# Optimization experiments

Measured on AMD Instinct MI355X. Metric: run time of the kernel, lower is better.

Reference implementation:

```python
import jax, jax.numpy as jnp
import numpy as np

H = 128
R = 14
B = 2048
TYPES = ['operator', 'table', 'column', 'predicate', 'operation', 'literal', 'numeral']
SIZES = {'operator': 100000, 'table': 20000, 'column': 120000, 'predicate': 60000,
         'operation': 100000, 'literal': 50000, 'numeral': 50000}
FEAT = {'operator': 4, 'table': 2, 'column': 10, 'predicate': 4, 'operation': 8,
        'literal': 1, 'numeral': 1}
# (name, src_type, dst_type, num_edges), order matches edge_type_mapping in the torch module
EDGES = [('ei_scannedby', 'table', 'operator', 100000),
         ('ei_pred_filters', 'predicate', 'operator', 100000),
         ('ei_outputby', 'column', 'operator', 100000),
         ('ei_col_connects', 'column', 'operation', 100000),
         ('ei_calledby', 'operator', 'operator', 100000),
         ('ei_op_filters', 'operation', 'operator', 100000),
         ('ei_op_connects', 'operation', 'predicate', 100000),
         ('ei_lit_connects', 'literal', 'operation', 100000),
         ('ei_num_connects', 'numeral', 'operation', 100000),
         ('ei_lit_self', 'literal', 'literal', 50000),
         ('ei_num_self', 'numeral', 'numeral', 50000),
         ('ei_tab_self', 'table', 'table', 20000),
         ('ei_col_self', 'column', 'column', 120000),
         ('ei_pred_self', 'predicate', 'predicate', 60000)]
OFFS = {}
_o = 0
for _t in TYPES:
    OFFS[_t] = _o
    _o += SIZES[_t]
N_TOTAL = _o


def setup_inputs():
    key = jax.random.key(0)
    ks = iter(jax.random.split(key, 64))
    inp = {}
    for t in TYPES:
        inp['x_' + t] = jax.random.normal(next(ks), (SIZES[t], FEAT[t]), jnp.float32)
    for name, s, d, E in EDGES:
        src = jax.random.randint(next(ks), (E,), 0, SIZES[s], jnp.int32)
        dst = jax.random.randint(next(ks), (E,), 0, SIZES[d], jnp.int32)
        inp[name] = jnp.stack([src, dst])
    inp['batch_operator'] = jnp.sort(
        jax.random.randint(next(ks), (SIZES['operator'],), 0, B, jnp.int32))

    def lin_w(k, din, dout):
        s = 1.0 / float(np.sqrt(din))
        return jax.random.uniform(k, (din, dout), jnp.float32, -s, s)

    for t in TYPES:
        inp['W_' + t] = lin_w(next(ks), FEAT[t], H)
        inp['b_' + t] = jnp.zeros((H,), jnp.float32)
    for c in ('c1', 'c2'):
        inp[c + '_root'] = lin_w(next(ks), H, H)
        inp[c + '_rel'] = jax.random.normal(next(ks), (R, H, H), jnp.float32) / float(np.sqrt(H))
        inp[c + '_bias'] = jnp.zeros((H,), jnp.float32)
    inp['n1_g'] = jnp.ones((H,), jnp.float32); inp['n1_b'] = jnp.zeros((H,), jnp.float32)
    inp['n2_g'] = jnp.ones((H,), jnp.float32); inp['n2_b'] = jnp.zeros((H,), jnp.float32)
    inp['W_lin'] = lin_w(next(ks), H, 1)
    inp['b_lin'] = jnp.zeros((1,), jnp.float32)
    return inp


def layer_norm(x, g, b, eps=1e-5):
    mu = jnp.mean(x, axis=-1, keepdims=True)
    var = jnp.var(x, axis=-1, keepdims=True)
    return (x - mu) * jax.lax.rsqrt(var + eps) * g + b


def rgcn(x, rel_edges, w_root, w_rel, bias):
    # PyG RGCNConv: root transform + per-relation gather -> GEMM -> scatter-mean into dst
    out = x @ w_root
    for r, (src, dst) in enumerate(rel_edges):
        msg = x[src] @ w_rel[r]  # [E_r, H]
        agg = jax.ops.segment_sum(msg, dst, num_segments=N_TOTAL)
        cnt = jax.ops.segment_sum(jnp.ones(src.shape, x.dtype), dst, num_segments=N_TOTAL)
        out = out + agg / jnp.maximum(cnt, 1.0)[:, None]
    return out + bias


def reference(x_operator, x_table, x_column, x_predicate, x_operation, x_literal, x_numeral,
              ei_scannedby, ei_pred_filters, ei_outputby, ei_col_connects, ei_calledby,
              ei_op_filters, ei_op_connects, ei_lit_connects, ei_num_connects, ei_lit_self,
              ei_num_self, ei_tab_self, ei_col_self, ei_pred_self, batch_operator,
              W_operator, b_operator, W_table, b_table, W_column, b_column,
              W_predicate, b_predicate, W_operation, b_operation, W_literal, b_literal,
              W_numeral, b_numeral, c1_root, c1_rel, c1_bias, c2_root, c2_rel, c2_bias,
              n1_g, n1_b, n2_g, n2_b, W_lin, b_lin):
    # per-node-type input embedding, then concat in fixed type order
    x = jnp.concatenate([
        x_operator @ W_operator + b_operator,
        x_table @ W_table + b_table,
        x_column @ W_column + b_column,
        x_predicate @ W_predicate + b_predicate,
        x_operation @ W_operation + b_operation,
        x_literal @ W_literal + b_literal,
        x_numeral @ W_numeral + b_numeral], axis=0)
    eis = [ei_scannedby, ei_pred_filters, ei_outputby, ei_col_connects, ei_calledby,
           ei_op_filters, ei_op_connects, ei_lit_connects, ei_num_connects, ei_lit_self,
           ei_num_self, ei_tab_self, ei_col_self, ei_pred_self]
    rel_edges = [(e[0] + OFFS[s], e[1] + OFFS[d]) for e, (_, s, d, _) in zip(eis, EDGES)]
    h = rgcn(x, rel_edges, c1_root, c1_rel, c1_bias)
    h = layer_norm(jax.nn.elu(h), n1_g, n1_b)  # dropout is identity in eval mode
    h = rgcn(h, rel_edges, c2_root, c2_rel, c2_bias)
    h = layer_norm(jax.nn.elu(h), n2_g, n2_b)
    op = h[:SIZES['operator']]  # operator offset is 0
    cnt = jax.ops.segment_sum(jnp.ones((op.shape[0],), op.dtype), batch_operator, num_segments=B)
    pooled = jax.ops.segment_sum(op, batch_operator, num_segments=B) / jnp.maximum(cnt, 1.0)[:, None]
    return (pooled @ W_lin + b_lin)[:, 0]  # [B]
```

## Files before the change

kernel.cpp:

```cpp
#include <hip/hip_runtime.h>
#include <hip/hip_bf16.h>
#include <math.h>

#define HD 128
#define N_OP 100000
#define N_L1 400000
#define NB 2048
#define CNT_TOT 1160000
#define EDG_TOT 1100000

typedef short short8 __attribute__((ext_vector_type(8)));
typedef float floatx4 __attribute__((ext_vector_type(4)));

static const int REL_E[14]    = {100000,100000,100000,100000,100000,100000,100000,100000,100000,50000,50000,20000,120000,60000};
static const int REL_DSZ[14]  = {100000,100000,100000,100000,100000,100000,60000,100000,100000,50000,50000,20000,120000,60000};
static const int CNT_OFF[14]  = {0,100000,200000,300000,400000,500000,600000,660000,760000,860000,910000,960000,980000,1100000};
static const int SRC_T[14] = {1,3,2,2,0,4,4,5,6,5,6,1,2,3};
static const int TF[7]  = {4,2,10,4,8,1,1};
static const size_t AGR_OFF[14] = {0,200000,600000,1600000,2600000,3000000,3800000,4280000,4380000,0,0,4480000,4520000,5720000};
#define AGR_TOT 5960000
static const int RELW[14] = {4,7,12,93,23,28,70,104,106,-1,-1,40,54,79};
static const int RELI[14] = {6,11,22,103,27,36,78,105,107,-1,-1,42,64,83};
static const int ROOTW[5] = {0,38,44,66,85};
static const int ROOTB[5] = {37,43,65,84,108};
#define WL1_ROWS 109

__device__ inline unsigned short f2bf(float f) {
  union { float f; unsigned int u; } v; v.f = f;
  unsigned int r = v.u + 0x7FFF + ((v.u >> 16) & 1);
  return (unsigned short)(r >> 16);
}
__device__ inline float bfu2f(unsigned short u) {
  union { unsigned int i; float f; } v; v.i = ((unsigned int)u) << 16; return v.f;
}

struct CJob { const int* dst; int coff; int E; int blk0; };
struct CombJob { const float* A; const float* bin; const float* Mtx; const float* extra; float* Wout; float* bout; int F; };
struct PrepPack {
  CJob j[12];
  int bblk0;
  int wstart;
  const int* batch; float* pcnt; int nop;
  CombJob c[17];
};

__global__ void prep_k(PrepPack P, const float* __restrict__ c2root,
                       const float* __restrict__ c2rel, __hip_bfloat16* __restrict__ Wt,
                       int* __restrict__ ICNT) {
  int b = blockIdx.x;
  if (b >= P.wstart) {
    int wj = b - P.wstart;
    if (wj < 17) {
      if (threadIdx.x >= 128) return;
      CombJob J = P.c[wj];
      int c = threadIdx.x;
      for (int f = 0; f <= J.F; ++f) {
        const float* arow = (f < J.F) ? &J.A[f * HD] : J.bin;
        float s = (f < J.F) ? 0.f : (J.extra ? J.extra[c] : 0.f);
        for (int k = 0; k < HD; ++k) s = fmaf(arow[k], J.Mtx[k * HD + c], s);
        if (f < J.F) J.Wout[f * HD + c] = s;
        else J.bout[c] = s;
      }
    } else {
      const int RID[6] = {-1, 0, 1, 2, 4, 5};
      int j = wj - 17;
      const float* W = (j == 0) ? c2root : (c2rel + (size_t)RID[j] * HD * HD);
      __hip_bfloat16* o = Wt + (size_t)j * 16384;
      for (int i = threadIdx.x; i < 16384; i += 256) {
        int i8 = i & 7;
        int ln = (i >> 3) & 63;
        int k4 = (i >> 9) & 3;
        int nt = i >> 11;
        int ln15 = ln & 15, quad = ln >> 4;
        int k = k4 * 32 + quad * 8 + i8;
        int n = nt * 16 + ln15;
        o[i] = __float2bfloat16(W[k * 128 + n]);
      }
    }
    return;
  }
  if (b >= P.bblk0) {
    int i = (b - P.bblk0) * 256 + threadIdx.x;
    if (i < P.nop) atomicAdd(&P.pcnt[P.batch[i]], 1.0f);
    return;
  }
  int ji = 0;
#pragma unroll
  for (int i = 1; i < 12; ++i) if (b >= P.j[i].blk0) ji = i;
  CJob J = P.j[ji];
  int e = (b - J.blk0) * 256 + threadIdx.x;
  if (e < J.E) atomicAdd(&ICNT[J.coff + J.dst[e]], 1);
}

#define SCAN_BLK 1024
__global__ void scan1(const int* __restrict__ in, int* __restrict__ out,
                      int* __restrict__ bsum, int n) {
  __shared__ int sh[256];
  int t = threadIdx.x;
  int base = blockIdx.x * SCAN_BLK + t * 4;
  int v0 = 0, v1 = 0, v2 = 0, v3 = 0;
  if (base + 3 < n) { int4 q = *(const int4*)&in[base]; v0 = q.x; v1 = q.y; v2 = q.z; v3 = q.w; }
  else {
    if (base < n) v0 = in[base];
    if (base + 1 < n) v1 = in[base + 1];
    if (base + 2 < n) v2 = in[base + 2];
    if (base + 3 < n) v3 = in[base + 3];
  }
  int ts = v0 + v1 + v2 + v3;
  sh[t] = ts; __syncthreads();
  for (int o = 1; o < 256; o <<= 1) {
    int x = (t >= o) ? sh[t - o] : 0;
    __syncthreads();
    sh[t] += x;
    __syncthreads();
  }
  int excl = sh[t] - ts;
  if (base < n) out[base] = excl;
  if (base + 1 < n) out[base + 1] = excl + v0;
  if (base + 2 < n) out[base + 2] = excl + v0 + v1;
  if (base + 3 < n) out[base + 3] = excl + v0 + v1 + v2;
  if (t == 255) bsum[blockIdx.x] = sh[255];
}

__global__ void scan3b(int* __restrict__ CUR, int2* __restrict__ OFF2,
                       const int* __restrict__ ICNT, const int* __restrict__ bs, int n) {
  __shared__ int sh[4];
  const int j = blockIdx.x, t = threadIdx.x;
  int s = 0;
  for (int i = t; i < j; i += 256) s += bs[i];
#pragma unroll
  for (int m = 32; m >= 1; m >>= 1) s += __shfl_xor(s, m, 64);
  if ((t & 63) == 0) sh[t >> 6] = s;
  __syncthreads();
  int base = sh[0] + sh[1] + sh[2] + sh[3];
  int i0 = j * SCAN_BLK + t * 4;
#pragma unroll
  for (int k = 0; k < 4; ++k) {
    int i = i0 + k;
    if (i < n) {
      int o = CUR[i] + base;
      CUR[i] = o;
      OFF2[i] = make_int2(o, ICNT[i]);
    }
  }
}

struct FJob { const int* src; const int* dst; int coff; int E; int blk0; };
struct FPackK { FJob j[12]; };

__global__ void fill_k(FPackK P, int* __restrict__ CUR, int* __restrict__ EDG) {
  int b = blockIdx.x;
  int ji = 0;
#pragma unroll
  for (int i = 1; i < 12; ++i) if (b >= P.j[i].blk0) ji = i;
  FJob J = P.j[ji];
  int e = (b - J.blk0) * 256 + threadIdx.x;
  if (e < J.E) {
    int pos = atomicAdd(&CUR[J.coff + J.dst[e]], 1);
    EDG[pos] = J.src[e];
  }
}

struct GJob { const float* x; float* agr; int coff; int D; int F; int blk0; };
struct GPack { GJob j[12]; };

template <int F>
__device__ inline void gathF(const float* __restrict__ x, float* __restrict__ agr,
                             const int* __restrict__ EDG, int2 oc, int d) {
  if (oc.y == 0) return;
  float s[F];
#pragma unroll
  for (int f = 0; f < F; ++f) s[f] = 0.f;
  for (int e = 0; e < oc.y; ++e) {
    int si = EDG[oc.x + e];
    const float* xp = &x[(size_t)si * F];
    if (F == 1) {
      s[0] += xp[0];
    } else if (F == 2) {
      float2 v = *(const float2*)xp; s[0] += v.x; s[1] += v.y;
    } else if (F == 4) {
      float4 v = *(const float4*)xp;
      s[0] += v.x; s[1] += v.y; s[2] += v.z; s[3] += v.w;
    } else if (F == 8) {
      float4 v0 = *(const float4*)xp, v1 = *(const float4*)(xp + 4);
      s[0] += v0.x; s[1] += v0.y; s[2] += v0.z; s[3] += v0.w;
      s[4] += v1.x; s[5] += v1.y; s[6] += v1.z; s[7] += v1.w;
    } else {
#pragma unroll
      for (int j = 0; j < F / 2; ++j) {
        float2 v = *(const float2*)(xp + 2 * j);
        s[2 * j] += v.x; s[2 * j + 1] += v.y;
      }
    }
  }
  float rc = 1.0f / (float)oc.y;
#pragma unroll
  for (int f = 0; f < F; ++f) s[f] *= rc;
  float* ap = &agr[(size_t)d * F];
  if (F == 1) { ap[0] = s[0]; }
  else if (F == 2) { *(float2*)ap = make_float2(s[0], s[1]); }
  else if (F == 4) { *(float4*)ap = make_float4(s[0], s[1], s[2], s[3]); }
  else if (F == 8) {
    *(float4*)ap = make_float4(s[0], s[1], s[2], s[3]);
    *(float4*)(ap + 4) = make_float4(s[4], s[5], s[6], s[7]);
  } else {
#pragma unroll
    for (int j = 0; j < F / 2; ++j)
      *(float2*)(ap + 2 * j) = make_float2(s[2 * j], s[2 * j + 1]);
  }
}

__global__ void gather_all(GPack P, const int2* __restrict__ OFF2, const int* __restrict__ EDG) {
  int b = blockIdx.x;
  int ji = 0;
#pragma unroll
  for (int i = 1; i < 12; ++i) if (b >= P.j[i].blk0) ji = i;
  GJob J = P.j[ji];
  int d = (b - J.blk0) * 256 + threadIdx.x;
  if (d >= J.D) return;
  int2 oc = OFF2[J.coff + d];
  switch (J.F) {
    case 1:  gathF<1>(J.x, J.agr, EDG, oc, d); break;
    case 2:  gathF<2>(J.x, J.agr, EDG, oc, d); break;
    case 4:  gathF<4>(J.x, J.agr, EDG, oc, d); break;
    case 8:  gathF<8>(J.x, J.agr, EDG, oc, d); break;
    default: gathF<10>(J.x, J.agr, EDG, oc, d); break;
  }
}

struct L1v2 {
  const float* x0; const float* x1; const float* x2; const float* x3; const float* x4;
  const float* AGR; const float* WL1; const int2* OFF2;
  const float* g; const float* b;
  unsigned short* Hb;
};

__device__ inline void ldv2(float* s, const float* __restrict__ p) {
  float2 v = *(const float2*)p; s[0] = v.x; s[1] = v.y;
}
__device__ inline void ldv4(float* s, const float* __restrict__ p) {
  float4 v = *(const float4*)p; s[0] = v.x; s[1] = v.y; s[2] = v.z; s[3] = v.w;
}
__device__ inline void relF1(float* s, const float* __restrict__ agr,
                             const int2* __restrict__ OFF2, int cb, int row) {
  if (OFF2[cb + row].y > 0) { s[0] = agr[row]; s[1] = 1.f; }
  else { s[0] = 0.f; s[1] = 0.f; }
}
__device__ inline void relF2(float* s, const float* __restrict__ agr,
                             const int2* __restrict__ OFF2, int cb, int row) {
  if (OFF2[cb + row].y > 0) { ldv2(s, &agr[(size_t)row * 2]); s[2] = 1.f; }
  else { s[0] = s[1] = s[2] = 0.f; }
}
__device__ inline void relF4(float* s, const float* __restrict__ agr,
                             const int2* __restrict__ OFF2, int cb, int row) {
  if (OFF2[cb + row].y > 0) { ldv4(s, &agr[(size_t)row * 4]); s[4] = 1.f; }
  else {
#pragma unroll
    for (int f = 0; f < 5; ++f) s[f] = 0.f;
  }
}
__device__ inline void relF8(float* s, const float* __restrict__ agr,
                             const int2* __restrict__ OFF2, int cb, int row) {
  if (OFF2[cb + row].y > 0) {
    ldv4(s, &agr[(size_t)row * 8]); ldv4(s + 4, &agr[(size_t)row * 8 + 4]); s[8] = 1.f;
  } else {
#pragma unroll
    for (int f = 0; f < 9; ++f) s[f] = 0.f;
  }
}
__device__ inline void relF10(float* s, const float* __restrict__ agr,
                              const int2* __restrict__ OFF2, int cb, int row) {
  if (OFF2[cb + row].y > 0) {
    const float* p = &agr[(size_t)row * 10];
#pragma unroll
    for (int j = 0; j < 5; ++j) ldv2(s + 2 * j, p + 2 * j);
    s[10] = 1.f;
  } else {
#pragma unroll
    for (int f = 0; f < 11; ++f) s[f] = 0.f;
  }
}

template <int KT>
__device__ inline void l1_dot8(const float* __restrict__ Ls, const float (&s)[KT],
                               int c4, float (&a)[8]) {
  {
    float4 w0 = *(const float4*)&Ls[KT * 128 + c4];
    float4 w1 = *(const float4*)&Ls[KT * 128 + c4 + 64];
    a[0] = w0.x; a[1] = w0.y; a[2] = w0.z; a[3] = w0.w;
    a[4] = w1.x; a[5] = w1.y; a[6] = w1.z; a[7] = w1.w;
  }
#pragma unroll
  for (int k = 0; k < KT; ++k) {
    float4 w0 = *(const float4*)&Ls[k * 128 + c4];
    float4 w1 = *(const float4*)&Ls[k * 128 + c4 + 64];
    a[0] = fmaf(s[k], w0.x, a[0]); a[1] = fmaf(s[k], w0.y, a[1]);
    a[2] = fmaf(s[k], w0.z, a[2]); a[3] = fmaf(s[k], w0.w, a[3]);
    a[4] = fmaf(s[k], w1.x, a[4]); a[5] = fmaf(s[k], w1.y, a[5]);
    a[6] = fmaf(s[k], w1.z, a[6]); a[7] = fmaf(s[k], w1.w, a[7]);
  }
}

__device__ inline void l1_fin8(float (&a)[8], int c4, const float* __restrict__ g,
                               const float* __restrict__ bb,
                               unsigned short* __restrict__ Hb, int orow) {
  float p = 0.f, q = 0.f;
#pragma unroll
  for (int j = 0; j < 8; ++j) {
    a[j] = (a[j] > 0.f) ? a[j] : (expf(a[j]) - 1.f);
    p += a[j]; q += a[j] * a[j];
  }
#pragma unroll
  for (int m = 8; m >= 1; m >>= 1) {
    p += __shfl_xor(p, m, 64);
    q += __shfl_xor(q, m, 64);
  }
  float mean = p * (1.0f / HD);
  float var = q * (1.0f / HD) - mean * mean;
  float rstd = rsqrtf(var + 1e-5f);
  float4 g0 = *(const float4*)&g[c4], g1 = *(const float4*)&g[c4 + 64];
  float4 b0 = *(const float4*)&bb[c4], b1 = *(const float4*)&bb[c4 + 64];
  float gg[8] = {g0.x, g0.y, g0.z, g0.w, g1.x, g1.y, g1.z, g1.w};
  float bv[8] = {b0.x, b0.y, b0.z, b0.w, b1.x, b1.y, b1.z, b1.w};
  float o[8];
#pragma unroll
  for (int j = 0; j < 8; ++j) o[j] = (a[j] - mean) * rstd * gg[j] + bv[j];
  uint2 lo, hi;
  lo.x = (unsigned int)f2bf(o[0]) | ((unsigned int)f2bf(o[1]) << 16);
  lo.y = (unsigned int)f2bf(o[2]) | ((unsigned int)f2bf(o[3]) << 16);
  hi.x = (unsigned int)f2bf(o[4]) | ((unsigned int)f2bf(o[5]) << 16);
  hi.y = (unsigned int)f2bf(o[6]) | ((unsigned int)f2bf(o[7]) << 16);
  *(uint2*)&Hb[(size_t)orow * HD + c4] = lo;
  *(uint2*)&Hb[(size_t)orow * HD + c4 + 64] = hi;
}

__global__ __launch_bounds__(256) void layer1_v5(L1v2 A) {
  __shared__ float Ls[38 * 128];
  const int b = blockIdx.x, t = threadIdx.x;
  const int wv = t >> 6, ln = t & 63;
  const int sub = ln >> 4, c4 = (ln & 15) * 4;
  int type, seg;
  if (b < 1563) { type = 0; seg = b; }
  else if (b < 1876) { type = 1; seg = b - 1563; }
  else if (b < 3751) { type = 2; seg = b - 1876; }
  else if (b < 4689) { type = 3; seg = b - 3751; }
  else { type = 4; seg = b - 4689; }
  const int NR[5] = {38, 6, 22, 19, 24};
  const int RB[5] = {0, 38, 44, 66, 85};
  const int TR[5] = {100000, 20000, 120000, 60000, 100000};
  const int OB[5] = {0, 100000, 120000, 240000, 300000};
  {
    const float4* src = (const float4*)(A.WL1 + RB[type] * 128);
    float4* dst = (float4*)Ls;
    int n4 = NR[type] * 32;
    for (int i = t; i < n4; i += 256) dst[i] = src[i];
  }
  __syncthreads();
  const int row0 = seg * 64, M = TR[type], ob = OB[type];

  if (type == 0) {
#pragma unroll
    for (int it = 0; it < 4; ++it) {
      int row = row0 + it * 16 + wv * 4 + sub;
      if (row >= M) continue;
      float s[37];
      ldv4(s, &A.x0[(size_t)row * 4]);
      relF2(s + 4, A.AGR + 0, A.OFF2, 0, row);
      relF4(s + 7, A.AGR + 200000, A.OFF2, 100000, row);
      relF10(s + 12, A.AGR + 600000, A.OFF2, 200000, row);
      relF4(s + 23, A.AGR + 2600000, A.OFF2, 400000, row);
      relF8(s + 28, A.AGR + 3000000, A.OFF2, 500000, row);
      float a[8];
      l1_dot8<37>(Ls, s, c4, a);
      l1_fin8(a, c4, A.g, A.b, A.Hb, ob + row);
    }
  } else if (type == 1) {
#pragma unroll
    for (int it = 0; it < 4; ++it) {
      int row = row0 + it * 16 + wv * 4 + sub;
      if (row >= M) continue;
      float s[5];
      ldv2(s, &A.x1[(size_t)row * 2]);
      relF2(s + 2, A.AGR + 4480000, A.OFF2, 960000, row);
      float a[8];
      l1_dot8<5>(Ls, s, c4, a);
      l1_fin8(a, c4, A.g, A.b, A.Hb, ob + row);
    }
  } else if (type == 2) {
#pragma unroll
    for (int it = 0; it < 4; ++it) {
      int row = row0 + it * 16 + wv * 4 + sub;
      if (row >= M) continue;
      float s[21];
      const float* p = &A.x2[(size_t)row * 10];
#pragma unroll
      for (int j = 0; j < 5; ++j) ldv2(s + 2 * j, p + 2 * j);
      relF10(s + 10, A.AGR + 4520000, A.OFF2, 980000, row);
      float a[8];
      l1_dot8<21>(Ls, s, c4, a);
      l1_fin8(a, c4, A.g, A.b, A.Hb, ob + row);
    }
  } else if (type == 3) {
#pragma unroll
    for (int it = 0; it < 4; ++it) {
      int row = row0 + it * 16 + wv * 4 + sub;
      if (row >= M) continue;
      float s[18];
      ldv4(s, &A.x3[(size_t)row * 4]);
      relF8(s + 4, A.AGR + 3800000, A.OFF2, 600000, row);
      relF4(s + 13, A.AGR + 5720000, A.OFF2, 1100000, row);
      float a[8];
      l1_dot8<18>(Ls, s, c4, a);
      l1_fin8(a, c4, A.g, A.b, A.Hb, ob + row);
    }
  } else {
#pragma unroll
    for (int it = 0; it < 4; ++it) {
      int row = row0 + it * 16 + wv * 4 + sub;
      if (row >= M) continue;
      float s[23];
      ldv4(s, &A.x4[(size_t)row * 8]);
      ldv4(s + 4, &A.x4[(size_t)row * 8 + 4]);
      relF10(s + 8, A.AGR + 1600000, A.OFF2, 300000, row);
      relF1(s + 19, A.AGR + 4280000, A.OFF2, 660000, row);
      relF1(s + 21, A.AGR + 4380000, A.OFF2, 760000, row);
      float a[8];
      l1_dot8<23>(Ls, s, c4, a);
      l1_fin8(a, c4, A.g, A.b, A.Hb, ob + row);
    }
  }
}

__global__ __launch_bounds__(256, 4)
void l2_fused(const unsigned short* __restrict__ Hb, const unsigned short* __restrict__ Wt,
              const int2* __restrict__ OFF2, const int* __restrict__ EDG,
              const float* __restrict__ c2bias, const float* __restrict__ n2g,
              const float* __restrict__ n2b, const float* __restrict__ Wl,
              const int* __restrict__ batch, float* __restrict__ accb, int M) {
  const int CSR_OFF[5] = {0, 100000, 200000, 400000, 500000};
  const int SOFF[5]    = {100000, 240000, 120000, 0, 300000};
  const int t = threadIdx.x, wv = t >> 6, ln = t & 63;
  const int quad = ln >> 4, ln15 = ln & 15, q8 = quad * 8;
  const int m0 = blockIdx.x * 64;
  const int rowA = m0 + wv * 16 + ln15;

  int2 ocs[5];
#pragma unroll
  for (int r = 0; r < 5; ++r)
    ocs[r] = (rowA < M) ? OFF2[CSR_OFF[r] + rowA] : make_int2(0, 0);
  int pre[5];
#pragma unroll
  for (int r = 0; r < 5; ++r)
    pre[r] = (ocs[r].y > 0) ? EDG[ocs[r].x] : 0;

  float bias_c[8], gw[8];
  float pg = 0.f, pb = 0.f;
#pragma unroll
  for (int nt = 0; nt < 8; ++nt) {
    int col = nt * 16 + ln15;
    float wl = Wl[col], gc = n2g[col], bc = n2b[col];
    bias_c[nt] = c2bias[col];
    gw[nt] = gc * wl;
    pg += gc * wl;
    pb += bc * wl;
  }
#pragma unroll
  for (int m = 8; m >= 1; m >>= 1) {
    pg += __shfl_xor(pg, m, 64);
    pb += __shfl_xor(pb, m, 64);
  }

  floatx4 acc[8];
#pragma unroll
  for (int b = 0; b < 8; ++b) acc[b] = (floatx4){0.f, 0.f, 0.f, 0.f};

  short8 nbuf[4];
  if (rowA < M) {
#pragma unroll
    for (int k4 = 0; k4 < 4; ++k4)
      nbuf[k4] = *(const short8*)&Hb[(size_t)rowA * HD + k4 * 32 + q8];
  } else {
#pragma unroll
    for (int k4 = 0; k4 < 4; ++k4)
#pragma unroll
      for (int j = 0; j < 8; ++j) nbuf[k4][j] = 0;
  }

#pragma unroll
  for (int term = 0; term < 6; ++term) {
    short8 afr[4];
#pragma unroll
    for (int k4 = 0; k4 < 4; ++k4) afr[k4] = nbuf[k4];

    if (term < 5) {
      int2 ocn = ocs[term];
      if (ocn.y > 0) {
        size_t s = (size_t)(pre[term] + SOFF[term]);
#pragma unroll
        for (int k4 = 0; k4 < 4; ++k4)
          nbuf[k4] = *(const short8*)&Hb[s * HD + k4 * 32 + q8];
      } else {
#pragma unroll
        for (int k4 = 0; k4 < 4; ++k4)
#pragma unroll
          for (int j = 0; j < 8; ++j) nbuf[k4][j] = 0;
      }
    }

    if (term > 0) {
      int2 oc = ocs[term - 1];
      if (oc.y > 1) {
        float sum[4][8];
#pragma unroll
        for (int k4 = 0; k4 < 4; ++k4)
#pragma unroll
          for (int j = 0; j < 8; ++j) sum[k4][j] = bfu2f((unsigned short)afr[k4][j]);
        int so = SOFF[term - 1];
        for (int e = 1; e < oc.y; ++e) {
          size_t s = (size_t)(EDG[oc.x + e] + so);
#pragma unroll
          for (int k4 = 0; k4 < 4; ++k4) {
            short8 h = *(const short8*)&Hb[s * HD + k4 * 32 + q8];
#pragma unroll
            for (int j = 0; j < 8; ++j) sum[k4][j] += bfu2f((unsigned short)h[j]);
          }
        }
        float rc = 1.0f / (float)oc.y;
#pragma unroll
        for (int k4 = 0; k4 < 4; ++k4)
#pragma unroll
          for (int j = 0; j < 8; ++j) afr[k4][j] = (short)f2bf(sum[k4][j] * rc);
      }
    }

    const unsigned short* wb = Wt + (size_t)term * 16384 + (size_t)ln * 8;
#pragma unroll
    for (int nt = 0; nt < 8; ++nt) {
      short8 b0 = *(const short8*)(wb + nt * 2048 + 0 * 512);
      short8 b1 = *(const short8*)(wb + nt * 2048 + 1 * 512);
      short8 b2 = *(const short8*)(wb + nt * 2048 + 2 * 512);
      short8 b3 = *(const short8*)(wb + nt * 2048 + 3 * 512);
      acc[nt] = __builtin_amdgcn_mfma_f32_16x16x32_bf16(afr[0], b0, acc[nt], 0, 0, 0);
      acc[nt] = __builtin_amdgcn_mfma_f32_16x16x32_bf16(afr[1], b1, acc[nt], 0, 0, 0);
      acc[nt] = __builtin_amdgcn_mfma_f32_16x16x32_bf16(afr[2], b2, acc[nt], 0, 0, 0);
      acc[nt] = __builtin_amdgcn_mfma_f32_16x16x32_bf16(afr[3], b3, acc[nt], 0, 0, 0);
    }
  }

#pragma unroll
  for (int r = 0; r < 4; ++r) {
    int rowD = m0 + wv * 16 + quad * 4 + r;
    float p = 0.f, q = 0.f, s1 = 0.f;
#pragma unroll
    for (int nt = 0; nt < 8; ++nt) {
      float v = acc[nt][r] + bias_c[nt];
      float e = (v > 0.f) ? v : (expf(v) - 1.f);
      p += e; q += e * e; s1 += e * gw[nt];
    }
#pragma unroll
    for (int m = 8; m >= 1; m >>= 1) {
      p += __shfl_xor(p, m, 64);
      q += __shfl_xor(q, m, 64);
      s1 += __shfl_xor(s1, m, 64);
    }
    if (ln15 == 0 && rowD < M) {
      float mean = p * (1.0f / HD);
      float var = q * (1.0f / HD) - mean * mean;
      float rstd = rsqrtf(var + 1e-5f);
      float o = rstd * (s1 - mean * pg) + pb;
      atomicAdd(&accb[batch[rowD]], o);
    }
  }
}

__global__ void final_kernel(const float* __restrict__ accb, const float* __restrict__ pcnt,
                             const float* __restrict__ bl, float* __restrict__ out) {
  int b = blockIdx.x * 256 + threadIdx.x;
  if (b < NB) out[b] = accb[b] / fmaxf(pcnt[b], 1.0f) + bl[0];
}

extern "C" void kernel_launch(void* const* d_in, const int* in_sizes, int n_in,
                              void* d_out, int out_size, void* d_ws, size_t ws_size,
                              hipStream_t stream) {
  const float* xt[7];
  for (int t = 0; t < 7; ++t) xt[t] = (const float*)d_in[t];
  const int* ei[14];
  for (int r = 0; r < 14; ++r) ei[r] = (const int*)d_in[7 + r];
  const int* batch = (const int*)d_in[21];
  const float* Wemb[7]; const float* bemb[7];
  for (int t = 0; t < 7; ++t) { Wemb[t] = (const float*)d_in[22 + 2 * t]; bemb[t] = (const float*)d_in[23 + 2 * t]; }
  const float* c_root[2] = {(const float*)d_in[36], (const float*)d_in[39]};
  const float* c_rel[2]  = {(const float*)d_in[37], (const float*)d_in[40]};
  const float* c_bias[2] = {(const float*)d_in[38], (const float*)d_in[41]};
  const float* ng[2] = {(const float*)d_in[42], (const float*)d_in[44]};
  const float* nbv[2] = {(const float*)d_in[43], (const float*)d_in[45]};
  const float* Wlin = (const float*)d_in[46];
  const float* blin = (const float*)d_in[47];
  float* out = (float*)d_out;

  char* base = (char*)d_ws;
  size_t off = 0;
  auto alloc = [&](size_t bytes) -> void* {
    void* p = base + off;
    off += (bytes + 255) & ~(size_t)255;
    return p;
  };
  __hip_bfloat16* Hb = (__hip_bfloat16*)alloc((size_t)N_L1 * HD * 2);
  float* AGR  = (float*)alloc((size_t)AGR_TOT * 4);
  int*   ICNT = (int*)alloc((size_t)CNT_TOT * 4 + (size_t)2 * NB * 4);
  float* ACC  = (float*)(ICNT + CNT_TOT);
  float* PCNT = ACC + NB;
  int*   CUR  = (int*)alloc((size_t)CNT_TOT * 4);
  int2*  OFF2 = (int2*)alloc((size_t)CNT_TOT * 8);
  int*   EDG  = (int*)alloc((size_t)EDG_TOT * 4);
  int*   BS   = (int*)alloc((size_t)1152 * 4);
  float* WL1  = (float*)alloc((size_t)WL1_ROWS * 128 * 4);
  __hip_bfloat16* WT3 = (__hip_bfloat16*)alloc((size_t)6 * 16384 * 2);

  static const int l1_rels[12] = {0,1,2,3,4,5,6,7,8,11,12,13};

  hipMemsetAsync(ICNT, 0, (size_t)CNT_TOT * 4 + (size_t)2 * NB * 4, stream);

  PrepPack PP;
  int blk = 0;
  for (int q = 0; q < 12; ++q) {
    int r = l1_rels[q];
    PP.j[q].dst = ei[r] + REL_E[r];
    PP.j[q].coff = CNT_OFF[r];
    PP.j[q].E = REL_E[r];
    PP.j[q].blk0 = blk;
    blk += (REL_E[r] + 255) / 256;
  }
  PP.bblk0 = blk; PP.batch = batch; PP.pcnt = PCNT; PP.nop = N_OP;
  blk += (N_OP + 255) / 256;
  PP.wstart = blk;
  for (int q = 0; q < 12; ++q) {
    int r = l1_rels[q]; int t = SRC_T[r];
    CombJob& J = PP.c[q];
    J.A = Wemb[t]; J.bin = bemb[t]; J.Mtx = c_rel[0] + (size_t)r * HD * HD;
    J.extra = nullptr;
    J.Wout = WL1 + (size_t)RELW[r] * 128;
    J.bout = WL1 + (size_t)RELI[r] * 128;
    J.F = TF[t];
  }
  for (int t = 0; t < 5; ++t) {
    CombJob& J = PP.c[12 + t];
    J.A = Wemb[t]; J.bin = bemb[t]; J.Mtx = c_root[0];
    J.extra = c_bias[0];
    J.Wout = WL1 + (size_t)ROOTW[t] * 128;
    J.bout = WL1 + (size_t)ROOTB[t] * 128;
    J.F = TF[t];
  }
  prep_k<<<blk + 23, 256, 0, stream>>>(PP, c_root[1], c_rel[1], WT3, ICNT);

  int nb1 = (CNT_TOT + SCAN_BLK - 1) / SCAN_BLK;
  scan1<<<nb1, 256, 0, stream>>>(ICNT, CUR, BS, CNT_TOT);
  scan3b<<<nb1, 256, 0, stream>>>(CUR, OFF2, ICNT, BS, CNT_TOT);

  FPackK FP;
  blk = 0;
  for (int q = 0; q < 12; ++q) {
    int r = l1_rels[q];
    FP.j[q].src = ei[r];
    FP.j[q].dst = ei[r] + REL_E[r];
    FP.j[q].coff = CNT_OFF[r];
    FP.j[q].E = REL_E[r];
    FP.j[q].blk0 = blk;
    blk += (REL_E[r] + 255) / 256;
  }
  fill_k<<<blk, 256, 0, stream>>>(FP, CUR, EDG);

  GPack GP;
  blk = 0;
  for (int q = 0; q < 12; ++q) {
    int r = l1_rels[q]; int t = SRC_T[r];
    GP.j[q].x = xt[t];
    GP.j[q].agr = AGR + AGR_OFF[r];
    GP.j[q].coff = CNT_OFF[r];
    GP.j[q].D = REL_DSZ[r];
    GP.j[q].F = TF[t];
    GP.j[q].blk0 = blk;
    blk += (REL_DSZ[r] + 255) / 256;
  }
  gather_all<<<blk, 256, 0, stream>>>(GP, OFF2, EDG);

  L1v2 A;
  A.x0 = xt[0]; A.x1 = xt[1]; A.x2 = xt[2]; A.x3 = xt[3]; A.x4 = xt[4];
  A.AGR = AGR; A.WL1 = WL1; A.OFF2 = OFF2;
  A.g = ng[0]; A.b = nbv[0]; A.Hb = (unsigned short*)Hb;
  layer1_v5<<<6252, 256, 0, stream>>>(A);

  l2_fused<<<(N_OP + 63) / 64, 256, 0, stream>>>(
      (const unsigned short*)Hb, (const unsigned short*)WT3,
      OFF2, EDG, c_bias[1], ng[1], nbv[1], Wlin, batch, ACC, N_OP);

  final_kernel<<<(NB + 255) / 256, 256, 0, stream>>>(ACC, PCNT, blin, out);
}
```

Before: 600.4 us.

## Replace CSR build with atomicExch linked-list adjacency

Result: no change. 598.9 us (-0.2%).

```diff
diff --git a/kernel.cpp b/kernel.cpp
--- a/kernel.cpp
+++ b/kernel.cpp
@@ -24,6 +24,7 @@
 static const int ROOTW[5] = {0,38,44,66,85};
 static const int ROOTB[5] = {37,43,65,84,108};
 #define WL1_ROWS 109
+static const int EOFF12[12] = {0,100000,200000,300000,400000,500000,600000,700000,800000,900000,920000,1040000};
 
 __device__ inline unsigned short f2bf(float f) {
   union { float f; unsigned int u; } v; v.f = f;
@@ -34,19 +35,19 @@
   union { unsigned int i; float f; } v; v.i = ((unsigned int)u) << 16; return v.f;
 }
 
-struct CJob { const int* dst; int coff; int E; int blk0; };
+struct XJob { const int* src; const int* dst; int coff; int eoff; int E; int blk0; };
 struct CombJob { const float* A; const float* bin; const float* Mtx; const float* extra; float* Wout; float* bout; int F; };
-struct PrepPack {
-  CJob j[12];
+struct XPack {
+  XJob j[12];
   int bblk0;
   int wstart;
   const int* batch; float* pcnt; int nop;
   CombJob c[17];
 };
 
-__global__ void prep_k(PrepPack P, const float* __restrict__ c2root,
+__global__ void exch_k(XPack P, const float* __restrict__ c2root,
                        const float* __restrict__ c2rel, __hip_bfloat16* __restrict__ Wt,
-                       int* __restrict__ ICNT) {
+                       int* __restrict__ HEAD, int2* __restrict__ SRCNXT) {
   int b = blockIdx.x;
   if (b >= P.wstart) {
     int wj = b - P.wstart;
@@ -87,77 +88,13 @@
   int ji = 0;
 #pragma unroll
   for (int i = 1; i < 12; ++i) if (b >= P.j[i].blk0) ji = i;
-  CJob J = P.j[ji];
-  int e = (b - J.blk0) * 256 + threadIdx.x;
-  if (e < J.E) atomicAdd(&ICNT[J.coff + J.dst[e]], 1);
-}
-
-#define SCAN_BLK 1024
-__global__ void scan1(const int* __restrict__ in, int* __restrict__ out,
-                      int* __restrict__ bsum, int n) {
-  __shared__ int sh[256];
-  int t = threadIdx.x;
-  int base = blockIdx.x * SCAN_BLK + t * 4;
-  int v0 = 0, v1 = 0, v2 = 0, v3 = 0;
-  if (base + 3 < n) { int4 q = *(const int4*)&in[base]; v0 = q.x; v1 = q.y; v2 = q.z; v3 = q.w; }
-  else {
-    if (base < n) v0 = in[base];
-    if (base + 1 < n) v1 = in[base + 1];
-    if (base + 2 < n) v2 = in[base + 2];
-    if (base + 3 < n) v3 = in[base + 3];
-  }
-  int ts = v0 + v1 + v2 + v3;
-  sh[t] = ts; __syncthreads();
-  for (int o = 1; o < 256; o <<= 1) {
-    int x = (t >= o) ? sh[t - o] : 0;
-    __syncthreads();
-    sh[t] += x;
-    __syncthreads();
-  }
-  int excl = sh[t] - ts;
-  if (base < n) out[base] = excl;
-  if (base + 1 < n) out[base + 1] = excl + v0;
-  if (base + 2 < n) out[base + 2] = excl + v0 + v1;
-  if (base + 3 < n) out[base + 3] = excl + v0 + v1 + v2;
-  if (t == 255) bsum[blockIdx.x] = sh[255];
-}
-
-__global__ void scan3b(int* __restrict__ CUR, int2* __restrict__ OFF2,
-                       const int* __restrict__ ICNT, const int* __restrict__ bs, int n) {
-  __shared__ int sh[4];
-  const int j = blockIdx.x, t = threadIdx.x;
-  int s = 0;
-  for (int i = t; i < j; i += 256) s += bs[i];
-#pragma unroll
-  for (int m = 32; m >= 1; m >>= 1) s += __shfl_xor(s, m, 64);
-  if ((t & 63) == 0) sh[t >> 6] = s;
-  __syncthreads();
-  int base = sh[0] + sh[1] + sh[2] + sh[3];
-  int i0 = j * SCAN_BLK + t * 4;
-#pragma unroll
-  for (int k = 0; k < 4; ++k) {
-    int i = i0 + k;
-    if (i < n) {
-      int o = CUR[i] + base;
-      CUR[i] = o;
-      OFF2[i] = make_int2(o, ICNT[i]);
-    }
-  }
-}
-
-struct FJob { const int* src; const int* dst; int coff; int E; int blk0; };
-struct FPackK { FJob j[12]; };
-
-__global__ void fill_k(FPackK P, int* __restrict__ CUR, int* __restrict__ EDG) {
-  int b = blockIdx.x;
-  int ji = 0;
-#pragma unroll
-  for (int i = 1; i < 12; ++i) if (b >= P.j[i].blk0) ji = i;
-  FJob J = P.j[ji];
+  XJob J = P.j[ji];
   int e = (b - J.blk0) * 256 + threadIdx.x;
   if (e < J.E) {
-    int pos = atomicAdd(&CUR[J.coff + J.dst[e]], 1);
-    EDG[pos] = J.src[e];
+    int d = J.dst[e];
+    int ge = J.eoff + e;
+    int old = atomicExch(&HEAD[J.coff + d], ge);
+    SRCNXT[ge] = make_int2(J.src[e], old);
   }
 }
 
@@ -166,14 +103,14 @@
 
 template <int F>
 __device__ inline void gathF(const float* __restrict__ x, float* __restrict__ agr,
-                             const int* __restrict__ EDG, int2 oc, int d) {
-  if (oc.y == 0) return;
+                             const int2* __restrict__ SRCNXT, int eg, int d) {
   float s[F];
 #pragma unroll
   for (int f = 0; f < F; ++f) s[f] = 0.f;
-  for (int e = 0; e < oc.y; ++e) {
-    int si = EDG[oc.x + e];
-    const float* xp = &x[(size_t)si * F];
+  int n = 0;
+  while (eg >= 0) {
+    int2 sn = SRCNXT[eg];
+    const float* xp = &x[(size_t)sn.x * F];
     if (F == 1) {
       s[0] += xp[0];
     } else if (F == 2) {
@@ -192,8 +129,10 @@
         s[2 * j] += v.x; s[2 * j + 1] += v.y;
       }
     }
-  }
-  float rc = 1.0f / (float)oc.y;
+    ++n;
+    eg = sn.y;
+  }
+  float rc = 1.0f / (float)n;
 #pragma unroll
   for (int f = 0; f < F; ++f) s[f] *= rc;
   float* ap = &agr[(size_t)d * F];
@@ -210,7 +149,8 @@
   }
 }
 
-__global__ void gather_all(GPack P, const int2* __restrict__ OFF2, const int* __restrict__ EDG) {
+__global__ void gather_all(GPack P, const int* __restrict__ HEAD,
+                           const int2* __restrict__ SRCNXT) {
   int b = blockIdx.x;
   int ji = 0;
 #pragma unroll
@@ -218,19 +158,20 @@
   GJob J = P.j[ji];
   int d = (b - J.blk0) * 256 + threadIdx.x;
   if (d >= J.D) return;
-  int2 oc = OFF2[J.coff + d];
+  int eg = HEAD[J.coff + d];
+  if (eg < 0) return;
   switch (J.F) {
-    case 1:  gathF<1>(J.x, J.agr, EDG, oc, d); break;
-    case 2:  gathF<2>(J.x, J.agr, EDG, oc, d); break;
-    case 4:  gathF<4>(J.x, J.agr, EDG, oc, d); break;
-    case 8:  gathF<8>(J.x, J.agr, EDG, oc, d); break;
-    default: gathF<10>(J.x, J.agr, EDG, oc, d); break;
+    case 1:  gathF<1>(J.x, J.agr, SRCNXT, eg, d); break;
+    case 2:  gathF<2>(J.x, J.agr, SRCNXT, eg, d); break;
+    case 4:  gathF<4>(J.x, J.agr, SRCNXT, eg, d); break;
+    case 8:  gathF<8>(J.x, J.agr, SRCNXT, eg, d); break;
+    default: gathF<10>(J.x, J.agr, SRCNXT, eg, d); break;
   }
 }
 
 struct L1v2 {
   const float* x0; const float* x1; const float* x2; const float* x3; const float* x4;
-  const float* AGR; const float* WL1; const int2* OFF2;
+  const float* AGR; const float* WL1; const int* HEAD;
   const float* g; const float* b;
   unsigned short* Hb;
 };
@@ -242,26 +183,26 @@
   float4 v = *(const float4*)p; s[0] = v.x; s[1] = v.y; s[2] = v.z; s[3] = v.w;
 }
 __device__ inline void relF1(float* s, const float* __restrict__ agr,
-                             const int2* __restrict__ OFF2, int cb, int row) {
-  if (OFF2[cb + row].y > 0) { s[0] = agr[row]; s[1] = 1.f; }
+                             const int* __restrict__ HEAD, int cb, int row) {
+  if (HEAD[cb + row] >= 0) { s[0] = agr[row]; s[1] = 1.f; }
   else { s[0] = 0.f; s[1] = 0.f; }
 }
 __device__ inline void relF2(float* s, const float* __restrict__ agr,
-                             const int2* __restrict__ OFF2, int cb, int row) {
-  if (OFF2[cb + row].y > 0) { ldv2(s, &agr[(size_t)row * 2]); s[2] = 1.f; }
+                             const int* __restrict__ HEAD, int cb, int row) {
+  if (HEAD[cb + row] >= 0) { ldv2(s, &agr[(size_t)row * 2]); s[2] = 1.f; }
   else { s[0] = s[1] = s[2] = 0.f; }
 }
 __device__ inline void relF4(float* s, const float* __restrict__ agr,
-                             const int2* __restrict__ OFF2, int cb, int row) {
-  if (OFF2[cb + row].y > 0) { ldv4(s, &agr[(size_t)row * 4]); s[4] = 1.f; }
+                             const int* __restrict__ HEAD, int cb, int row) {
+  if (HEAD[cb + row] >= 0) { ldv4(s, &agr[(size_t)row * 4]); s[4] = 1.f; }
   else {
 #pragma unroll
     for (int f = 0; f < 5; ++f) s[f] = 0.f;
   }
 }
 __device__ inline void relF8(float* s, const float* __restrict__ agr,
-                             const int2* __restrict__ OFF2, int cb, int row) {
-  if (OFF2[cb + row].y > 0) {
+                             const int* __restrict__ HEAD, int cb, int row) {
+  if (HEAD[cb + row] >= 0) {
     ldv4(s, &agr[(size_t)row * 8]); ldv4(s + 4, &agr[(size_t)row * 8 + 4]); s[8] = 1.f;
   } else {
 #pragma unroll
@@ -269,8 +210,8 @@
   }
 }
 __device__ inline void relF10(float* s, const float* __restrict__ agr,
-                              const int2* __restrict__ OFF2, int cb, int row) {
-  if (OFF2[cb + row].y > 0) {
+                              const int* __restrict__ HEAD, int cb, int row) {
+  if (HEAD[cb + row] >= 0) {
     const float* p = &agr[(size_t)row * 10];
 #pragma unroll
     for (int j = 0; j < 5; ++j) ldv2(s + 2 * j, p + 2 * j);
@@ -365,11 +306,11 @@
       if (row >= M) continue;
       float s[37];
       ldv4(s, &A.x0[(size_t)row * 4]);
-      relF2(s + 4, A.AGR + 0, A.OFF2, 0, row);
-      relF4(s + 7, A.AGR + 200000, A.OFF2, 100000, row);
-      relF10(s + 12, A.AGR + 600000, A.OFF2, 200000, row);
-      relF4(s + 23, A.AGR + 2600000, A.OFF2, 400000, row);
-      relF8(s + 28, A.AGR + 3000000, A.OFF2, 500000, row);
+      relF2(s + 4, A.AGR + 0, A.HEAD, 0, row);
+      relF4(s + 7, A.AGR + 200000, A.HEAD, 100000, row);
+      relF10(s + 12, A.AGR + 600000, A.HEAD, 200000, row);
+      relF4(s + 23, A.AGR + 2600000, A.HEAD, 400000, row);
+      relF8(s + 28, A.AGR + 3000000, A.HEAD, 500000, row);
       float a[8];
       l1_dot8<37>(Ls, s, c4, a);
       l1_fin8(a, c4, A.g, A.b, A.Hb, ob + row);
@@ -381,7 +322,7 @@
       if (row >= M) continue;
       float s[5];
       ldv2(s, &A.x1[(size_t)row * 2]);
-      relF2(s + 2, A.AGR + 4480000, A.OFF2, 960000, row);
+      relF2(s + 2, A.AGR + 4480000, A.HEAD, 960000, row);
       float a[8];
       l1_dot8<5>(Ls, s, c4, a);
       l1_fin8(a, c4, A.g, A.b, A.Hb, ob + row);
@@ -395,7 +336,7 @@
       const float* p = &A.x2[(size_t)row * 10];
 #pragma unroll
       for (int j = 0; j < 5; ++j) ldv2(s + 2 * j, p + 2 * j);
-      relF10(s + 10, A.AGR + 4520000, A.OFF2, 980000, row);
+      relF10(s + 10, A.AGR + 4520000, A.HEAD, 980000, row);
       float a[8];
       l1_dot8<21>(Ls, s, c4, a);
       l1_fin8(a, c4, A.g, A.b, A.Hb, ob + row);
@@ -407,8 +348,8 @@
       if (row >= M) continue;
       float s[18];
       ldv4(s, &A.x3[(size_t)row * 4]);
-      relF8(s + 4, A.AGR + 3800000, A.OFF2, 600000, row);
-      relF4(s + 13, A.AGR + 5720000, A.OFF2, 1100000, row);
+      relF8(s + 4, A.AGR + 3800000, A.HEAD, 600000, row);
+      relF4(s + 13, A.AGR + 5720000, A.HEAD, 1100000, row);
       float a[8];
       l1_dot8<18>(Ls, s, c4, a);
       l1_fin8(a, c4, A.g, A.b, A.Hb, ob + row);
@@ -421,9 +362,9 @@
       float s[23];
       ldv4(s, &A.x4[(size_t)row * 8]);
       ldv4(s + 4, &A.x4[(size_t)row * 8 + 4]);
-      relF10(s + 8, A.AGR + 1600000, A.OFF2, 300000, row);
-      relF1(s + 19, A.AGR + 4280000, A.OFF2, 660000, row);
-      relF1(s + 21, A.AGR + 4380000, A.OFF2, 760000, row);
+      relF10(s + 8, A.AGR + 1600000, A.HEAD, 300000, row);
+      relF1(s + 19, A.AGR + 4280000, A.HEAD, 660000, row);
+      relF1(s + 21, A.AGR + 4380000, A.HEAD, 760000, row);
       float a[8];
       l1_dot8<23>(Ls, s, c4, a);
       l1_fin8(a, c4, A.g, A.b, A.Hb, ob + row);
@@ -433,7 +374,7 @@
 
 __global__ __launch_bounds__(256, 4)
 void l2_fused(const unsigned short* __restrict__ Hb, const unsigned short* __restrict__ Wt,
-              const int2* __restrict__ OFF2, const int* __restrict__ EDG,
+              const int* __restrict__ HEAD, const int2* __restrict__ SRCNXT,
               const float* __restrict__ c2bias, const float* __restrict__ n2g,
               const float* __restrict__ n2b, const float* __restrict__ Wl,
               const int* __restrict__ batch, float* __restrict__ accb, int M) {
@@ -444,14 +385,14 @@
   const int m0 = blockIdx.x * 64;
   const int rowA = m0 + wv * 16 + ln15;
 
-  int2 ocs[5];
+  int hd[5];
 #pragma unroll
   for (int r = 0; r < 5; ++r)
-    ocs[r] = (rowA < M) ? OFF2[CSR_OFF[r] + rowA] : make_int2(0, 0);
-  int pre[5];
+    hd[r] = (rowA < M) ? HEAD[CSR_OFF[r] + rowA] : -1;
+  int2 sn[5];
 #pragma unroll
   for (int r = 0; r < 5; ++r)
-    pre[r] = (ocs[r].y > 0) ? EDG[ocs[r].x] : 0;
+    sn[r] = (hd[r] >= 0) ? SRCNXT[hd[r]] : make_int2(0, -1);
 
   float bias_c[8], gw[8];
   float pg = 0.f, pb = 0.f;
@@ -493,9 +434,8 @@
     for (int k4 = 0; k4 < 4; ++k4) afr[k4] = nbuf[k4];
 
     if (term < 5) {
-      int2 ocn = ocs[term];
-      if (ocn.y > 0) {
-        size_t s = (size_t)(pre[term] + SOFF[term]);
+      if (hd[term] >= 0) {
+        size_t s = (size_t)(sn[term].x + SOFF[term]);
 #pragma unroll
         for (int k4 = 0; k4 < 4; ++k4)
           nbuf[k4] = *(const short8*)&Hb[s * HD + k4 * 32 + q8];
@@ -508,24 +448,29 @@
     }
 
     if (term > 0) {
-      int2 oc = ocs[term - 1];
-      if (oc.y > 1) {
+      int r = term - 1;
+      if (hd[r] >= 0 && sn[r].y >= 0) {
         float sum[4][8];
 #pragma unroll
         for (int k4 = 0; k4 < 4; ++k4)
 #pragma unroll
           for (int j = 0; j < 8; ++j) sum[k4][j] = bfu2f((unsigned short)afr[k4][j]);
-        int so = SOFF[term - 1];
-        for (int e = 1; e < oc.y; ++e) {
-          size_t s = (size_t)(EDG[oc.x + e] + so);
+        int so = SOFF[r];
+        int n = 1;
+        int eg = sn[r].y;
+        while (eg >= 0) {
+          int2 s2 = SRCNXT[eg];
+          size_t s = (size_t)(s2.x + so);
 #pragma unroll
           for (int k4 = 0; k4 < 4; ++k4) {
             short8 h = *(const short8*)&Hb[s * HD + k4 * 32 + q8];
 #pragma unroll
             for (int j = 0; j < 8; ++j) sum[k4][j] += bfu2f((unsigned short)h[j]);
           }
+          ++n;
+          eg = s2.y;
         }
-        float rc = 1.0f / (float)oc.y;
+        float rc = 1.0f / (float)n;
 #pragma unroll
         for (int k4 = 0; k4 < 4; ++k4)
 #pragma unroll
@@ -607,36 +552,36 @@
   };
   __hip_bfloat16* Hb = (__hip_bfloat16*)alloc((size_t)N_L1 * HD * 2);
   float* AGR  = (float*)alloc((size_t)AGR_TOT * 4);
-  int*   ICNT = (int*)alloc((size_t)CNT_TOT * 4 + (size_t)2 * NB * 4);
-  float* ACC  = (float*)(ICNT + CNT_TOT);
+  int*   HEAD = (int*)alloc((size_t)CNT_TOT * 4);
+  float* ACC  = (float*)alloc((size_t)2 * NB * 4);
   float* PCNT = ACC + NB;
-  int*   CUR  = (int*)alloc((size_t)CNT_TOT * 4);
-  int2*  OFF2 = (int2*)alloc((size_t)CNT_TOT * 8);
-  int*   EDG  = (int*)alloc((size_t)EDG_TOT * 4);
-  int*   BS   = (int*)alloc((size_t)1152 * 4);
+  int2*  SRCNXT = (int2*)alloc((size_t)EDG_TOT * 8);
   float* WL1  = (float*)alloc((size_t)WL1_ROWS * 128 * 4);
   __hip_bfloat16* WT3 = (__hip_bfloat16*)alloc((size_t)6 * 16384 * 2);
 
   static const int l1_rels[12] = {0,1,2,3,4,5,6,7,8,11,12,13};
 
-  hipMemsetAsync(ICNT, 0, (size_t)CNT_TOT * 4 + (size_t)2 * NB * 4, stream);
-
-  PrepPack PP;
+  hipMemsetAsync(HEAD, 0xFF, (size_t)CNT_TOT * 4, stream);
+  hipMemsetAsync(ACC, 0, (size_t)2 * NB * 4, stream);
+
+  XPack XP;
   int blk = 0;
   for (int q = 0; q < 12; ++q) {
     int r = l1_rels[q];
-    PP.j[q].dst = ei[r] + REL_E[r];
-    PP.j[q].coff = CNT_OFF[r];
-    PP.j[q].E = REL_E[r];
-    PP.j[q].blk0 = blk;
+    XP.j[q].src = ei[r];
+    XP.j[q].dst = ei[r] + REL_E[r];
+    XP.j[q].coff = CNT_OFF[r];
+    XP.j[q].eoff = EOFF12[q];
+    XP.j[q].E = REL_E[r];
+    XP.j[q].blk0 = blk;
     blk += (REL_E[r] + 255) / 256;
   }
-  PP.bblk0 = blk; PP.batch = batch; PP.pcnt = PCNT; PP.nop = N_OP;
+  XP.bblk0 = blk; XP.batch = batch; XP.pcnt = PCNT; XP.nop = N_OP;
   blk += (N_OP + 255) / 256;
-  PP.wstart = blk;
+  XP.wstart = blk;
   for (int q = 0; q < 12; ++q) {
     int r = l1_rels[q]; int t = SRC_T[r];
-    CombJob& J = PP.c[q];
+    CombJob& J = XP.c[q];
     J.A = Wemb[t]; J.bin = bemb[t]; J.Mtx = c_rel[0] + (size_t)r * HD * HD;
     J.extra = nullptr;
     J.Wout = WL1 + (size_t)RELW[r] * 128;
@@ -644,31 +589,14 @@
     J.F = TF[t];
   }
   for (int t = 0; t < 5; ++t) {
-    CombJob& J = PP.c[12 + t];
+    CombJob& J = XP.c[12 + t];
     J.A = Wemb[t]; J.bin = bemb[t]; J.Mtx = c_root[0];
     J.extra = c_bias[0];
     J.Wout = WL1 + (size_t)ROOTW[t] * 128;
     J.bout = WL1 + (size_t)ROOTB[t] * 128;
     J.F = TF[t];
   }
-  prep_k<<<blk + 23, 256, 0, stream>>>(PP, c_root[1], c_rel[1], WT3, ICNT);
-
-  int nb1 = (CNT_TOT + SCAN_BLK - 1) / SCAN_BLK;
-  scan1<<<nb1, 256, 0, stream>>>(ICNT, CUR, BS, CNT_TOT);
-  scan3b<<<nb1, 256, 0, stream>>>(CUR, OFF2, ICNT, BS, CNT_TOT);
-
-  FPackK FP;
-  blk = 0;
-  for (int q = 0; q < 12; ++q) {
-    int r = l1_rels[q];
-    FP.j[q].src = ei[r];
-    FP.j[q].dst = ei[r] + REL_E[r];
-    FP.j[q].coff = CNT_OFF[r];
-    FP.j[q].E = REL_E[r];
-    FP.j[q].blk0 = blk;
-    blk += (REL_E[r] + 255) / 256;
-  }
-  fill_k<<<blk, 256, 0, stream>>>(FP, CUR, EDG);
+  exch_k<<<blk + 23, 256, 0, stream>>>(XP, c_root[1], c_rel[1], WT3, HEAD, SRCNXT);
 
   GPack GP;
   blk = 0;
@@ -682,17 +610,17 @@
     GP.j[q].blk0 = blk;
     blk += (REL_DSZ[r] + 255) / 256;
   }
-  gather_all<<<blk, 256, 0, stream>>>(GP, OFF2, EDG);
+  gather_all<<<blk, 256, 0, stream>>>(GP, HEAD, SRCNXT);
 
   L1v2 A;
   A.x0 = xt[0]; A.x1 = xt[1]; A.x2 = xt[2]; A.x3 = xt[3]; A.x4 = xt[4];
-  A.AGR = AGR; A.WL1 = WL1; A.OFF2 = OFF2;
+  A.AGR = AGR; A.WL1 = WL1; A.HEAD = HEAD;
   A.g = ng[0]; A.b = nbv[0]; A.Hb = (unsigned short*)Hb;
   layer1_v5<<<6252, 256, 0, stream>>>(A);
 
   l2_fused<<<(N_OP + 63) / 64, 256, 0, stream>>>(
       (const unsigned short*)Hb, (const unsigned short*)WT3,
-      OFF2, EDG, c_bias[1], ng[1], nbv[1], Wlin, batch, ACC, N_OP);
+      HEAD, SRCNXT, c_bias[1], ng[1], nbv[1], Wlin, batch, ACC, N_OP);
 
   final_kernel<<<(NB + 255) / 256, 256, 0, stream>>>(ACC, PCNT, blin, out);
 }
```
